# Kernel tuning notes

Measured on AMD Instinct MI355X. Metric: run time of the kernel, lower is better.

Reference implementation:

```python
import jax, jax.numpy as jnp
import numpy as np

TEMPERATURE = 0.07
NORM_EPS = 1e-12   # F.normalize eps
LOG_EPS = 1e-08


def setup_inputs() -> dict:
    key = jax.random.key(0)
    k1, k2 = jax.random.split(key)
    N, D, C = 8192, 512, 64
    projections = jax.random.normal(k1, (N, D), dtype=jnp.float32)
    targets = jax.random.randint(k2, (N,), 0, C, dtype=jnp.int64)
    return {"projections": projections, "targets": targets}


def reference(projections, targets):
    # L2-normalize rows (matches F.normalize: x / max(||x||, eps))
    norm = jnp.linalg.norm(projections, axis=1, keepdims=True)
    p = projections / jnp.maximum(norm, NORM_EPS)

    # [N, N] cosine similarity / temperature
    sim = jnp.matmul(p, p.T) / TEMPERATURE
    # row-max subtraction for numerical stability (gradient flows through max,
    # as in the torch original)
    sim = sim - jnp.max(sim, axis=1, keepdims=True)
    exp_sim = jnp.exp(sim)

    n = projections.shape[0]
    eye = jnp.eye(n, dtype=bool)
    mask_self = ~eye                                   # exclude self-pairs
    mask_pos = (targets[:, None] == targets[None, :]) & mask_self

    denom = jnp.sum(jnp.where(mask_self, exp_sim, 0.0), axis=1, keepdims=True)
    log_prob = sim - jnp.log(denom + LOG_EPS)

    num = jnp.sum(jnp.where(mask_pos, log_prob, 0.0), axis=1)
    cnt = jnp.sum(mask_pos, axis=1).astype(log_prob.dtype)
    # divide_no_nan: 0 where cnt == 0
    loss_per_sample = jnp.where(cnt == 0, 0.0, num / jnp.where(cnt == 0, 1.0, cnt))
    return loss_per_sample
```

## Files before the change

kernel.cpp:

```cpp
#include <hip/hip_runtime.h>
#include <hip/hip_bf16.h>
#include <math.h>

#define N_ROWS 8192
#define DIM    512
#define NCLS   64
#define BM     256
#define BK     64
#define NKT    (DIM / BK)
#define NTILE  (N_ROWS / BM)
#define NTRI   (NTILE * (NTILE + 1) / 2)
#define NSLOT  NTILE
#define M_CONST 14.285714285714286f
#define L2E     1.4426950408889634f
#define M2_CONST 20.60992915555662f
#define SCALE2  4.539815541256959f

using bf16x8 = __attribute__((ext_vector_type(8))) short;
using f32x4  = __attribute__((ext_vector_type(4))) float;

static __device__ inline unsigned short f2bf(float x) {
  unsigned u = __float_as_uint(x);
  unsigned r = u + 0x7FFFu + ((u >> 16) & 1u);
  return (unsigned short)(r >> 16);
}

__global__ __launch_bounds__(256) void normalize_rows(const float* __restrict__ proj,
                                                      unsigned short* __restrict__ outb) {
  const int row  = blockIdx.x * 4 + (threadIdx.x >> 6);
  const int lane = threadIdx.x & 63;
  const float4* src = (const float4*)(proj + (size_t)row * DIM);
  float4 a = src[lane * 2];
  float4 b = src[lane * 2 + 1];
  float ss = a.x*a.x + a.y*a.y + a.z*a.z + a.w*a.w
           + b.x*b.x + b.y*b.y + b.z*b.z + b.w*b.w;
#pragma unroll
  for (int off = 1; off < 64; off <<= 1) ss += __shfl_xor(ss, off);
  const float scale = SCALE2 / fmaxf(sqrtf(ss), 1e-12f);
  float v[8] = {a.x, a.y, a.z, a.w, b.x, b.y, b.z, b.w};
  unsigned short h[8];
#pragma unroll
  for (int i = 0; i < 8; ++i) h[i] = f2bf(v[i] * scale);
  uint4 packed;
  packed.x = (unsigned)h[0] | ((unsigned)h[1] << 16);
  packed.y = (unsigned)h[2] | ((unsigned)h[3] << 16);
  packed.z = (unsigned)h[4] | ((unsigned)h[5] << 16);
  packed.w = (unsigned)h[6] | ((unsigned)h[7] << 16);
  *(uint4*)(outb + (size_t)row * DIM + lane * 8) = packed;
}

__global__ __launch_bounds__(1024) void class_hist(const int* __restrict__ tgt,
                                                   int* __restrict__ hist) {
  __shared__ int h[16][NCLS];
  const int wid = threadIdx.x >> 6;
  const int lane = threadIdx.x & 63;
  if (lane < NCLS) h[wid][lane] = 0;
  __syncthreads();
  for (int i = threadIdx.x; i < N_ROWS; i += 1024) atomicAdd(&h[wid][tgt[i]], 1);
  __syncthreads();
  if (threadIdx.x < NCLS) {
    int s = 0;
#pragma unroll
    for (int w = 0; w < 16; ++w) s += h[w][threadIdx.x];
    hist[threadIdx.x] = s;
  }
}

__global__ __launch_bounds__(512) void supcon_tile(const unsigned short* __restrict__ p16,
                                                   const int* __restrict__ tgt,
                                                   float* __restrict__ dpart,
                                                   float* __restrict__ spart) {
  const int logical = ((int)blockIdx.x & 7) * (NTRI / 8) + ((int)blockIdx.x >> 3);
  int rem = logical, br = 0;
  while (rem >= NTILE - br) { rem -= NTILE - br; ++br; }
  const int bc = br + rem;

  __shared__ short As[2][BM * BK];
  __shared__ short Bs[2][BM * BK];
  __shared__ int   tgr[BM], tgc[BM];
  __shared__ float redE[4][BM], redS[4][BM];
  __shared__ float redEc[2][BM], redSc[2][BM];

  const int tid  = threadIdx.x;
  const int lane = tid & 63;
  const int wid  = tid >> 6;
  const int wm = wid >> 2, wn = wid & 3;
  const int lhi = lane >> 4, llo = lane & 15;

  const size_t rowA0 = (size_t)br * BM;
  const size_t rowB0 = (size_t)bc * BM;

#define STAGE_ARR(XS, BUF, ROW0, KT) do {                                       \
  _Pragma("unroll")                                                             \
  for (int j = 0; j < 4; ++j) {                                                 \
    const int g  = tid + j * 512;                                               \
    const int r  = g >> 3, gp = g & 7;                                          \
    const int gl = gp ^ (r & 7);                                                \
    const unsigned short* src = p16 + ((ROW0) + r) * DIM + (KT) * BK + gl * 8;  \
    __builtin_amdgcn_global_load_lds((const __attribute__((address_space(1))) void*)src, \
        (__attribute__((address_space(3))) void*)&XS[BUF][g * 8], 16, 0, 0);    \
  }                                                                             \
} while (0)

  STAGE_ARR(As, 0, rowA0, 0);
  STAGE_ARR(Bs, 0, rowB0, 0);
  if (tid < BM) tgr[tid] = tgt[br * BM + tid];
  else          tgc[tid - BM] = tgt[bc * BM + (tid - BM)];

  f32x4 zero = {0.f, 0.f, 0.f, 0.f};
  f32x4 acc[8][4];
#pragma unroll
  for (int i = 0; i < 8; ++i)
#pragma unroll
    for (int j = 0; j < 4; ++j) acc[i][j] = zero;

  __syncthreads();

#pragma unroll
  for (int kt = 0; kt < NKT; ++kt) {
    const int cur = kt & 1, nxt = cur ^ 1;
#pragma unroll
    for (int ph = 0; ph < 4; ++ph) {
      const int mh = ph >> 1, nh = ph & 1;

      bf16x8 af[4][2], bf[2][2];
#pragma unroll
      for (int mi = 0; mi < 4; ++mi) {
        const int Ra = wm * 128 + mh * 64 + mi * 16 + llo;
#pragma unroll
        for (int ks = 0; ks < 2; ++ks)
          af[mi][ks] = *(const bf16x8*)&As[cur][Ra * BK + (((ks * 4 + lhi) ^ (Ra & 7)) * 8)];
      }
#pragma unroll
      for (int ni = 0; ni < 2; ++ni) {
        const int Rb = wn * 64 + nh * 32 + ni * 16 + llo;
#pragma unroll
        for (int ks = 0; ks < 2; ++ks)
          bf[ni][ks] = *(const bf16x8*)&Bs[cur][Rb * BK + (((ks * 4 + lhi) ^ (Rb & 7)) * 8)];
      }

      if (kt + 1 < NKT) {
        if (ph == 0)      STAGE_ARR(As, nxt, rowA0, kt + 1);
        else if (ph == 1) STAGE_ARR(Bs, nxt, rowB0, kt + 1);
      }

      __builtin_amdgcn_s_barrier();
      asm volatile("s_waitcnt lgkmcnt(0)" ::: "memory");
      __builtin_amdgcn_sched_barrier(0);
      __builtin_amdgcn_s_setprio(1);
#pragma unroll
      for (int ks = 0; ks < 2; ++ks)
#pragma unroll
        for (int mi = 0; mi < 4; ++mi)
#pragma unroll
          for (int ni = 0; ni < 2; ++ni)
            acc[mh * 4 + mi][nh * 2 + ni] =
                __builtin_amdgcn_mfma_f32_16x16x32_bf16(af[mi][ks], bf[ni][ks],
                                                        acc[mh * 4 + mi][nh * 2 + ni], 0, 0, 0);
      __builtin_amdgcn_s_setprio(0);
      if (ph == 3) {
        asm volatile("s_waitcnt vmcnt(0)" ::: "memory");
        __builtin_amdgcn_sched_barrier(0);
      }
      __builtin_amdgcn_s_barrier();
    }
  }
#undef STAGE_ARR

  const bool diag = (br == bc);
  int tc[4];
#pragma unroll
  for (int ni = 0; ni < 4; ++ni) tc[ni] = tgc[wn * 64 + ni * 16 + llo];
  float ecol[4] = {0.f, 0.f, 0.f, 0.f};
  float scol[4] = {0.f, 0.f, 0.f, 0.f};

#pragma unroll
  for (int mi = 0; mi < 8; ++mi) {
#pragma unroll
    for (int rg = 0; rg < 4; ++rg) {
      const int rin  = wm * 128 + mi * 16 + lhi * 4 + rg;
      const int trow = tgr[rin];
      float esum = 0.f, ssum = 0.f;
#pragma unroll
      for (int ni = 0; ni < 4; ++ni) {
        const int cin = wn * 64 + ni * 16 + llo;
        const float x = acc[mi][ni][rg];
        const bool self = diag && (rin == cin);
        const float e = self ? 0.f : __builtin_amdgcn_exp2f(x - M2_CONST);
        const bool pos = (!self) && (trow == tc[ni]);
        const float sv = pos ? x : 0.f;
        esum += e;  ssum += sv;
        ecol[ni] += e;  scol[ni] += sv;
      }
#pragma unroll
      for (int off = 1; off < 16; off <<= 1) {
        esum += __shfl_xor(esum, off);
        ssum += __shfl_xor(ssum, off);
      }
      if (llo == 0) { redE[wn][rin] = esum; redS[wn][rin] = ssum; }
    }
  }
  if (!diag) {
#pragma unroll
    for (int ni = 0; ni < 4; ++ni) {
      float ec = ecol[ni], sc = scol[ni];
      ec += __shfl_xor(ec, 16); ec += __shfl_xor(ec, 32);
      sc += __shfl_xor(sc, 16); sc += __shfl_xor(sc, 32);
      if (lhi == 0) {
        redEc[wm][wn * 64 + ni * 16 + llo] = ec;
        redSc[wm][wn * 64 + ni * 16 + llo] = sc;
      }
    }
  }
  __syncthreads();

  if (tid < BM) {
    const float e = redE[0][tid] + redE[1][tid] + redE[2][tid] + redE[3][tid];
    const float s = redS[0][tid] + redS[1][tid] + redS[2][tid] + redS[3][tid];
    dpart[(size_t)bc * N_ROWS + rowA0 + tid] = e;
    spart[(size_t)bc * N_ROWS + rowA0 + tid] = s;
  } else if (!diag) {
    const int c = tid - BM;
    dpart[(size_t)br * N_ROWS + rowB0 + c] = redEc[0][c] + redEc[1][c];
    spart[(size_t)br * N_ROWS + rowB0 + c] = redSc[0][c] + redSc[1][c];
  }
}

__global__ __launch_bounds__(256) void combine_loss(const float* __restrict__ dpart,
                                                    const float* __restrict__ spart,
                                                    const int* __restrict__ tgt,
                                                    const int* __restrict__ hist,
                                                    float* __restrict__ out) {
  __shared__ float dsh[4][64], ssh[4][64];
  const int lane = threadIdx.x & 63;
  const int g    = threadIdx.x >> 6;
  const int r    = blockIdx.x * 64 + lane;
  float d = 0.f, s = 0.f;
  for (int k = g * (NSLOT / 4); k < (g + 1) * (NSLOT / 4); ++k) {
    d += dpart[(size_t)k * N_ROWS + r];
    s += spart[(size_t)k * N_ROWS + r];
  }
  dsh[g][lane] = d; ssh[g][lane] = s;
  __syncthreads();
  if (g == 0) {
    d = dsh[0][lane] + dsh[1][lane] + dsh[2][lane] + dsh[3][lane];
    s = ssh[0][lane] + ssh[1][lane] + ssh[2][lane] + ssh[3][lane];
    const int cnt = hist[tgt[r]] - 1;
    out[r] = (cnt > 0) ? (s / (L2E * (float)cnt) - M_CONST - logf(d + 1e-8f)) : 0.f;
  }
}

extern "C" void kernel_launch(void* const* d_in, const int* in_sizes, int n_in,
                              void* d_out, int out_size, void* d_ws, size_t ws_size,
                              hipStream_t stream) {
  const float* proj = (const float*)d_in[0];
  const int*   tgt  = (const int*)d_in[1];
  float* out = (float*)d_out;

  char* ws = (char*)d_ws;
  unsigned short* p16  = (unsigned short*)ws;
  float* dpart = (float*)(ws + (size_t)8 * 1024 * 1024);
  float* spart = (float*)(ws + (size_t)9 * 1024 * 1024);
  int*   hist  = (int*)(ws + (size_t)10 * 1024 * 1024);

  normalize_rows<<<N_ROWS / 4, 256, 0, stream>>>(proj, p16);
  class_hist<<<1, 1024, 0, stream>>>(tgt, hist);
  supcon_tile<<<NTRI, 512, 0, stream>>>(p16, tgt, dpart, spart);
  combine_loss<<<N_ROWS / 64, 256, 0, stream>>>(dpart, spart, tgt, hist, out);
}
```

Baseline: 107.0 us.

## Restructure GEMM k-loop into two halves with one barrier per k-tile

Replaces the four-phase inner loop, which had two barriers per phase, with two half-phases per k-tile. All B fragments are loaded once and reused across both M halves, both global stages are issued up front, and a single barrier closes each k-tile. It also pins occupancy to two waves per EU with an attribute so the compiler can use more registers. The intent is to cut barrier count and LDS fragment reloads. The cost is more live registers and less interleaving between the staging writes and the MFMA phases.

```diff
diff --git a/kernel.cpp b/kernel.cpp
--- a/kernel.cpp
+++ b/kernel.cpp
@@ -66,6 +66,7 @@
   }
 }
 
+__attribute__((amdgpu_waves_per_eu(2, 2)))
 __global__ __launch_bounds__(512) void supcon_tile(const unsigned short* __restrict__ p16,
                                                    const int* __restrict__ tgt,
                                                    float* __restrict__ dpart,
@@ -119,51 +120,63 @@
 #pragma unroll
   for (int kt = 0; kt < NKT; ++kt) {
     const int cur = kt & 1, nxt = cur ^ 1;
-#pragma unroll
-    for (int ph = 0; ph < 4; ++ph) {
-      const int mh = ph >> 1, nh = ph & 1;
-
-      bf16x8 af[4][2], bf[2][2];
-#pragma unroll
-      for (int mi = 0; mi < 4; ++mi) {
-        const int Ra = wm * 128 + mh * 64 + mi * 16 + llo;
-#pragma unroll
-        for (int ks = 0; ks < 2; ++ks)
-          af[mi][ks] = *(const bf16x8*)&As[cur][Ra * BK + (((ks * 4 + lhi) ^ (Ra & 7)) * 8)];
-      }
-#pragma unroll
-      for (int ni = 0; ni < 2; ++ni) {
-        const int Rb = wn * 64 + nh * 32 + ni * 16 + llo;
-#pragma unroll
-        for (int ks = 0; ks < 2; ++ks)
-          bf[ni][ks] = *(const bf16x8*)&Bs[cur][Rb * BK + (((ks * 4 + lhi) ^ (Rb & 7)) * 8)];
-      }
-
-      if (kt + 1 < NKT) {
-        if (ph == 0)      STAGE_ARR(As, nxt, rowA0, kt + 1);
-        else if (ph == 1) STAGE_ARR(Bs, nxt, rowB0, kt + 1);
-      }
-
-      __builtin_amdgcn_s_barrier();
-      asm volatile("s_waitcnt lgkmcnt(0)" ::: "memory");
-      __builtin_amdgcn_sched_barrier(0);
-      __builtin_amdgcn_s_setprio(1);
+
+    bf16x8 bf[4][2], af[4][2];
+#pragma unroll
+    for (int ni = 0; ni < 4; ++ni) {
+      const int Rb = wn * 64 + ni * 16 + llo;
 #pragma unroll
       for (int ks = 0; ks < 2; ++ks)
-#pragma unroll
-        for (int mi = 0; mi < 4; ++mi)
-#pragma unroll
-          for (int ni = 0; ni < 2; ++ni)
-            acc[mh * 4 + mi][nh * 2 + ni] =
-                __builtin_amdgcn_mfma_f32_16x16x32_bf16(af[mi][ks], bf[ni][ks],
-                                                        acc[mh * 4 + mi][nh * 2 + ni], 0, 0, 0);
-      __builtin_amdgcn_s_setprio(0);
-      if (ph == 3) {
-        asm volatile("s_waitcnt vmcnt(0)" ::: "memory");
-        __builtin_amdgcn_sched_barrier(0);
-      }
-      __builtin_amdgcn_s_barrier();
-    }
+        bf[ni][ks] = *(const bf16x8*)&Bs[cur][Rb * BK + (((ks * 4 + lhi) ^ (Rb & 7)) * 8)];
+    }
+#pragma unroll
+    for (int mi = 0; mi < 4; ++mi) {
+      const int Ra = wm * 128 + mi * 16 + llo;
+#pragma unroll
+      for (int ks = 0; ks < 2; ++ks)
+        af[mi][ks] = *(const bf16x8*)&As[cur][Ra * BK + (((ks * 4 + lhi) ^ (Ra & 7)) * 8)];
+    }
+    if (kt + 1 < NKT) {
+      STAGE_ARR(As, nxt, rowA0, kt + 1);
+      STAGE_ARR(Bs, nxt, rowB0, kt + 1);
+    }
+    asm volatile("s_waitcnt lgkmcnt(0)" ::: "memory");
+    __builtin_amdgcn_sched_barrier(0);
+    __builtin_amdgcn_s_setprio(1);
+#pragma unroll
+    for (int ks = 0; ks < 2; ++ks)
+#pragma unroll
+      for (int mi = 0; mi < 4; ++mi)
+#pragma unroll
+        for (int ni = 0; ni < 4; ++ni)
+          acc[mi][ni] = __builtin_amdgcn_mfma_f32_16x16x32_bf16(af[mi][ks], bf[ni][ks],
+                                                                acc[mi][ni], 0, 0, 0);
+    __builtin_amdgcn_s_setprio(0);
+
+    bf16x8 ag[4][2];
+#pragma unroll
+    for (int mi = 0; mi < 4; ++mi) {
+      const int Ra = wm * 128 + 64 + mi * 16 + llo;
+#pragma unroll
+      for (int ks = 0; ks < 2; ++ks)
+        ag[mi][ks] = *(const bf16x8*)&As[cur][Ra * BK + (((ks * 4 + lhi) ^ (Ra & 7)) * 8)];
+    }
+    asm volatile("s_waitcnt lgkmcnt(0)" ::: "memory");
+    __builtin_amdgcn_sched_barrier(0);
+    __builtin_amdgcn_s_setprio(1);
+#pragma unroll
+    for (int ks = 0; ks < 2; ++ks)
+#pragma unroll
+      for (int mi = 0; mi < 4; ++mi)
+#pragma unroll
+        for (int ni = 0; ni < 4; ++ni)
+          acc[4 + mi][ni] = __builtin_amdgcn_mfma_f32_16x16x32_bf16(ag[mi][ks], bf[ni][ks],
+                                                                    acc[4 + mi][ni], 0, 0, 0);
+    __builtin_amdgcn_s_setprio(0);
+
+    asm volatile("s_waitcnt vmcnt(0)" ::: "memory");
+    __builtin_amdgcn_sched_barrier(0);
+    __builtin_amdgcn_s_barrier();
   }
 #undef STAGE_ARR
 
```

New measurement: 99.20 us. 7.3% less time.
